# Performance work log

Hardware: AMD Instinct MI355X
Metric: run time of the kernel (lower is better)

The kernel has to match this reference:

```python
import jax, jax.numpy as jnp
import numpy as np

IN_DIM, BANDS = 42, 22
H_VAD, H_NOISE, H_DEN = 24, 48, 96


def gru(x, w_ih, w_hh, b_ih, b_hh):
    """torch.nn.GRU (batch_first) semantics, h0=0.
    x: [B,T,D]; w_ih: [3H,D]; w_hh: [3H,H]; gate order r,z,n."""
    H = w_hh.shape[1]
    # precompute input projections for all timesteps (big GEMM, recurrence only on H)
    xp = jnp.einsum('btd,gd->btg', x, w_ih) + b_ih  # [B,T,3H]

    def step(h, xt):
        hp = h @ w_hh.T + b_hh
        xr, xz, xn = jnp.split(xt, 3, axis=-1)
        hr, hz, hn = jnp.split(hp, 3, axis=-1)
        r = jax.nn.sigmoid(xr + hr)
        z = jax.nn.sigmoid(xz + hz)
        n = jnp.tanh(xn + r * hn)
        h_new = (1.0 - z) * n + z * h
        return h_new, h_new

    h0 = jnp.zeros((x.shape[0], H), x.dtype)
    _, hs = jax.lax.scan(step, h0, jnp.swapaxes(xp, 0, 1))  # [T,B,H]
    return jnp.swapaxes(hs, 0, 1)  # [B,T,H]


def setup_inputs() -> dict:
    key = jax.random.key(0)
    ks = jax.random.split(key, 20)

    def w(k, shape, fan):
        return (jax.random.normal(k, shape, jnp.float32) / np.sqrt(fan)).astype(jnp.float32)

    B, T = 256, 2000
    d_noise_in = H_VAD + H_VAD + IN_DIM     # 90
    d_den_in = H_VAD + H_NOISE + IN_DIM     # 114
    return {
        'x': jax.random.normal(ks[0], (B, T, IN_DIM), jnp.float32),
        'in_w': w(ks[1], (H_VAD, IN_DIM), IN_DIM),
        'in_b': jnp.zeros((H_VAD,), jnp.float32),
        'vad_wih': w(ks[2], (3 * H_VAD, H_VAD), H_VAD),
        'vad_whh': w(ks[3], (3 * H_VAD, H_VAD), H_VAD),
        'vad_bih': jnp.zeros((3 * H_VAD,), jnp.float32),
        'vad_bhh': jnp.zeros((3 * H_VAD,), jnp.float32),
        'vad_out_w': w(ks[4], (1, H_VAD), H_VAD),
        'vad_out_b': jnp.zeros((1,), jnp.float32),
        'noise_wih': w(ks[5], (3 * H_NOISE, d_noise_in), d_noise_in),
        'noise_whh': w(ks[6], (3 * H_NOISE, H_NOISE), H_NOISE),
        'noise_bih': jnp.zeros((3 * H_NOISE,), jnp.float32),
        'noise_bhh': jnp.zeros((3 * H_NOISE,), jnp.float32),
        'den_wih': w(ks[7], (3 * H_DEN, d_den_in), d_den_in),
        'den_whh': w(ks[8], (3 * H_DEN, H_DEN), H_DEN),
        'den_bih': jnp.zeros((3 * H_DEN,), jnp.float32),
        'den_bhh': jnp.zeros((3 * H_DEN,), jnp.float32),
        'out_w': w(ks[9], (BANDS, H_DEN), H_DEN),
        'out_b': jnp.zeros((BANDS,), jnp.float32),
    }


def reference(x, in_w, in_b, vad_wih, vad_whh, vad_bih, vad_bhh,
              vad_out_w, vad_out_b, noise_wih, noise_whh, noise_bih, noise_bhh,
              den_wih, den_whh, den_bih, den_bhh, out_w, out_b):
    tmp = jnp.tanh(jnp.einsum('btd,hd->bth', x, in_w) + in_b)          # [B,T,24]
    vad_h = gru(tmp, vad_wih, vad_whh, vad_bih, vad_bhh)               # [B,T,24]
    vad = jax.nn.sigmoid(jnp.einsum('bth,oh->bto', vad_h, vad_out_w) + vad_out_b)
    noise_in = jnp.concatenate([tmp, vad_h, x], axis=-1)               # [B,T,90]
    noise_h = gru(noise_in, noise_wih, noise_whh, noise_bih, noise_bhh)  # [B,T,48]
    den_in = jnp.concatenate([vad_h, noise_h, x], axis=-1)             # [B,T,114]
    den_h = gru(den_in, den_wih, den_whh, den_bih, den_bhh)            # [B,T,96]
    gains = jax.nn.sigmoid(jnp.einsum('bth,oh->bto', den_h, out_w) + out_b)
    return gains, vad
```

## Files before the change

kernel.cpp:

```cpp
#include <hip/hip_runtime.h>

typedef _Float16 f16;
typedef _Float16 h2 __attribute__((ext_vector_type(2)));
typedef unsigned int u32;

#define TB  256
#define TTT 2000
#define INW 42
#define HV  24
#define HN  48
#define HD  96
#define NTH 640

__device__ __forceinline__ float fsigm(float v) {
    return __builtin_amdgcn_rcpf(1.0f + __builtin_amdgcn_exp2f(-1.44269504089f * v));
}
__device__ __forceinline__ float ftanh(float v) {
    float e = __builtin_amdgcn_exp2f(2.88539008178f * v);
    return 1.0f - 2.0f * __builtin_amdgcn_rcpf(e + 1.0f);
}
__device__ __forceinline__ float dot2f(u32 a, u32 w, float c) {
#if __has_builtin(__builtin_amdgcn_fdot2)
    return __builtin_amdgcn_fdot2(__builtin_bit_cast(h2, a), __builtin_bit_cast(h2, w), c, false);
#else
    h2 av = __builtin_bit_cast(h2, a), wv = __builtin_bit_cast(h2, w);
    return c + (float)av[0] * (float)wv[0] + (float)av[1] * (float)wv[1];
#endif
}
__device__ __forceinline__ u32 packw(float a, float b) {
    h2 v; v[0] = (f16)a; v[1] = (f16)b;
    return __builtin_bit_cast(u32, v);
}
template<int CTRL>
__device__ __forceinline__ float dpp_add(float x) {
    int y = __builtin_amdgcn_mov_dpp(__builtin_bit_cast(int, x), CTRL, 0xF, 0xF, true);
    return x + __builtin_bit_cast(float, y);
}

#define SYNCB() asm volatile("s_waitcnt lgkmcnt(0)\n\ts_barrier" ::: "memory")

#define ACCI(AV, W, IDX) do { u32 _a = (AV); \
    rr = dot2f(_a, W[0][IDX], rr); zz = dot2f(_a, W[1][IDX], zz); an = dot2f(_a, W[2][IDX], an); } while (0)
#define ACCH(AV, W, IDX) do { u32 _a = (AV); \
    rr = dot2f(_a, W[0][IDX], rr); zz = dot2f(_a, W[1][IDX], zz); hn = dot2f(_a, W[2][IDX], hn); } while (0)
#define RED4_Q() do { \
    rr = dpp_add<0xB1>(rr); rr = dpp_add<0x4E>(rr); \
    zz = dpp_add<0xB1>(zz); zz = dpp_add<0x4E>(zz); \
    an = dpp_add<0xB1>(an); an = dpp_add<0x4E>(an); \
    hn = dpp_add<0xB1>(hn); hn = dpp_add<0x4E>(hn); } while (0)
#define RED4_1() do { \
    rr = dpp_add<0xB1>(rr); zz = dpp_add<0xB1>(zz); \
    an = dpp_add<0xB1>(an); hn = dpp_add<0xB1>(hn); } while (0)

template<int N> struct IC { static constexpr int val = N; };

__global__ __launch_bounds__(NTH, 3) void rnnoise_kernel(
    const float* __restrict__ gx,
    const float* __restrict__ in_w,      const float* __restrict__ in_b,
    const float* __restrict__ vad_wih,   const float* __restrict__ vad_whh,
    const float* __restrict__ vad_bih,   const float* __restrict__ vad_bhh,
    const float* __restrict__ vad_out_w, const float* __restrict__ vad_out_b,
    const float* __restrict__ noise_wih, const float* __restrict__ noise_whh,
    const float* __restrict__ noise_bih, const float* __restrict__ noise_bhh,
    const float* __restrict__ den_wih,   const float* __restrict__ den_whh,
    const float* __restrict__ den_bih,   const float* __restrict__ den_bhh,
    const float* __restrict__ out_w,     const float* __restrict__ out_b,
    float* __restrict__ gains, float* __restrict__ vout)
{
    __shared__ __align__(16) f16 s_x[4][48];
    __shared__ __align__(16) f16 s_tmp[4][24];
    __shared__ __align__(16) f16 s_vadh[4][24];
    __shared__ __align__(16) f16 s_noih[4][48];
    __shared__ __align__(16) f16 s_denh[4][96];

    const int tid  = threadIdx.x;
    const int wid  = tid >> 6;
    const int lane = tid & 63;
    const int b    = blockIdx.x;

    if (tid < 96)  ((u32*)s_x)[tid]    = 0u;
    if (tid < 48)  ((u32*)s_tmp)[tid]  = 0u;
    if (tid < 48)  ((u32*)s_vadh)[tid] = 0u;
    if (tid < 96)  ((u32*)s_noih)[tid] = 0u;
    if (tid < 192) ((u32*)s_denh)[tid] = 0u;
    __syncthreads();

    const int role = (wid == 9) ? 2 : ((wid == 4 || wid == 5 || wid == 8) ? 1 : 0);

    if (role == 0) {
        const int dwi = (wid < 4) ? wid : (wid - 2);
        const int u = dwi * 16 + (lane >> 2), q = lane & 3;
        u32 wdh[3][12], wdx[3][6], wdv[3][3], wdn[3][6];
        #pragma unroll
        for (int g = 0; g < 3; ++g) {
            const float* wr = den_whh + (g * HD + u) * HD + 24 * q;
            #pragma unroll
            for (int j = 0; j < 12; ++j) wdh[g][j] = packw(wr[2*j], wr[2*j+1]);
            const float* wi = den_wih + (g * HD + u) * 114;
            #pragma unroll
            for (int j = 0; j < 6; ++j) {
                int c0 = 12*q + 2*j;
                float a = (c0     < INW) ? wi[72 + c0]     : 0.f;
                float c = (c0 + 1 < INW) ? wi[72 + c0 + 1] : 0.f;
                wdx[g][j] = packw(a, c);
            }
            #pragma unroll
            for (int j = 0; j < 3; ++j) wdv[g][j] = packw(wi[6*q + 2*j], wi[6*q + 2*j + 1]);
            #pragma unroll
            for (int j = 0; j < 6; ++j) wdn[g][j] = packw(wi[24 + 12*q + 2*j], wi[24 + 12*q + 2*j + 1]);
        }
        const float bdr  = den_bih[u]      + den_bhh[u];
        const float bdz  = den_bih[HD+u]   + den_bhh[HD+u];
        const float bdni = den_bih[2*HD+u];
        const float bdnh = den_bhh[2*HD+u];
        float hreg = 0.f;

        auto step = [&](auto PC, int k) {
            constexpr int P  = decltype(PC)::val;
            constexpr int SI = (P + 1) & 3;
            if (k >= 3 && k <= TTT + 2) {
                float rr = 0, zz = 0, an = 0, hn = 0;
                const uint4* hp = (const uint4*)&s_denh[P][24*q];
                #pragma unroll
                for (int v = 0; v < 3; ++v) {
                    uint4 a = hp[v];
                    ACCH(a.x, wdh, 4*v+0); ACCH(a.y, wdh, 4*v+1);
                    ACCH(a.z, wdh, 4*v+2); ACCH(a.w, wdh, 4*v+3);
                }
                const uint2* xp = (const uint2*)&s_x[SI][12*q];
                #pragma unroll
                for (int v = 0; v < 3; ++v) { uint2 a = xp[v]; ACCI(a.x, wdx, 2*v); ACCI(a.y, wdx, 2*v+1); }
                const u32* vp = (const u32*)&s_vadh[SI][6*q];
                #pragma unroll
                for (int v = 0; v < 3; ++v) ACCI(vp[v], wdv, v);
                const uint2* np = (const uint2*)&s_noih[SI][12*q];
                #pragma unroll
                for (int v = 0; v < 3; ++v) { uint2 a = np[v]; ACCI(a.x, wdn, 2*v); ACCI(a.y, wdn, 2*v+1); }
                RED4_Q();
                if (q == 0) {
                    float r = fsigm(rr + bdr);
                    float z = fsigm(zz + bdz);
                    float n = ftanh(an + bdni + r * (hn + bdnh));
                    hreg = z * (hreg - n) + n;
                    s_denh[SI][u] = (f16)hreg;
                }
            }
            SYNCB();
        };
        #pragma clang loop unroll(disable)
        for (int k0 = 0; k0 < TTT + 4; k0 += 4) {
            step(IC<0>{}, k0); step(IC<1>{}, k0+1); step(IC<2>{}, k0+2); step(IC<3>{}, k0+3);
        }

    } else if (role == 1) {
        const int nwi = (wid == 4) ? 0 : ((wid == 5) ? 1 : 2);
        const int L = nwi * 64 + lane, u = L >> 2, q = L & 3;
        const int o = L >> 3, s8 = L & 7;
        const int oc = (o < 22) ? o : 0;
        u32 wnh[3][6], wnt[3][3], wnv[3][3], wnx[3][6], wo[6];
        #pragma unroll
        for (int g = 0; g < 3; ++g) {
            const float* wr = noise_whh + (g * HN + u) * HN + 12 * q;
            #pragma unroll
            for (int j = 0; j < 6; ++j) wnh[g][j] = packw(wr[2*j], wr[2*j+1]);
            const float* wi = noise_wih + (g * HN + u) * 90;
            #pragma unroll
            for (int j = 0; j < 3; ++j) wnt[g][j] = packw(wi[6*q + 2*j], wi[6*q + 2*j + 1]);
            #pragma unroll
            for (int j = 0; j < 3; ++j) wnv[g][j] = packw(wi[24 + 6*q + 2*j], wi[24 + 6*q + 2*j + 1]);
            #pragma unroll
            for (int j = 0; j < 6; ++j) {
                int c0 = 12*q + 2*j;
                float a = (c0     < INW) ? wi[48 + c0]     : 0.f;
                float c = (c0 + 1 < INW) ? wi[48 + c0 + 1] : 0.f;
                wnx[g][j] = packw(a, c);
            }
        }
        #pragma unroll
        for (int j = 0; j < 6; ++j) wo[j] = packw(out_w[oc*HD + 12*s8 + 2*j], out_w[oc*HD + 12*s8 + 2*j + 1]);
        const float bnr  = noise_bih[u]    + noise_bhh[u];
        const float bnz  = noise_bih[HN+u] + noise_bhh[HN+u];
        const float bnni = noise_bih[2*HN+u];
        const float bnnh = noise_bhh[2*HN+u];
        const float bo   = out_b[oc];
        float hreg = 0.f;

        auto step = [&](auto PC, int k) {
            constexpr int P  = decltype(PC)::val;
            constexpr int SI = (P + 2) & 3;
            constexpr int SH = (P + 1) & 3;
            if (k >= 2 && k <= TTT + 1) {
                float rr = 0, zz = 0, an = 0, hn = 0;
                const uint2* hp = (const uint2*)&s_noih[SH][12*q];
                #pragma unroll
                for (int v = 0; v < 3; ++v) { uint2 a = hp[v]; ACCH(a.x, wnh, 2*v); ACCH(a.y, wnh, 2*v+1); }
                const u32* tp = (const u32*)&s_tmp[SI][6*q];
                #pragma unroll
                for (int v = 0; v < 3; ++v) ACCI(tp[v], wnt, v);
                const u32* vp = (const u32*)&s_vadh[SI][6*q];
                #pragma unroll
                for (int v = 0; v < 3; ++v) ACCI(vp[v], wnv, v);
                const uint2* xp = (const uint2*)&s_x[SI][12*q];
                #pragma unroll
                for (int v = 0; v < 3; ++v) { uint2 a = xp[v]; ACCI(a.x, wnx, 2*v); ACCI(a.y, wnx, 2*v+1); }
                RED4_Q();
                if (q == 0) {
                    float r = fsigm(rr + bnr);
                    float z = fsigm(zz + bnz);
                    float n = ftanh(an + bnni + r * (hn + bnnh));
                    hreg = z * (hreg - n) + n;
                    s_noih[SI][u] = (f16)hreg;
                }
            }
            if (k >= 4) {
                float acc = 0;
                const uint2* dp = (const uint2*)&s_denh[P][12*s8];
                #pragma unroll
                for (int v = 0; v < 3; ++v) {
                    uint2 a = dp[v];
                    acc = dot2f(a.x, wo[2*v], acc); acc = dot2f(a.y, wo[2*v+1], acc);
                }
                acc = dpp_add<0xB1>(acc); acc = dpp_add<0x4E>(acc);
                acc += __shfl_xor(acc, 4);
                if (s8 == 0 && o < 22)
                    gains[((size_t)b * TTT + (k - 4)) * 22 + o] = fsigm(acc + bo);
            }
            SYNCB();
        };
        #pragma clang loop unroll(disable)
        for (int k0 = 0; k0 < TTT + 4; k0 += 4) {
            step(IC<0>{}, k0); step(IC<1>{}, k0+1); step(IC<2>{}, k0+2); step(IC<3>{}, k0+3);
        }

    } else {
        const int l = lane;
        const int u = (l < 48) ? (l >> 1) : 0, q2 = l & 1;
        u32 wvi[3][6], wvh[3][6], wtm[12];
        float bvr = 0, bvz = 0, bvni = 0, bvnh = 0, btm = 0, wvo_u = 0;
        if (l < 48) {
            #pragma unroll
            for (int g = 0; g < 3; ++g) {
                const float* wi = vad_wih + (g * HV + u) * HV + 12 * q2;
                const float* wh = vad_whh + (g * HV + u) * HV + 12 * q2;
                #pragma unroll
                for (int j = 0; j < 6; ++j) {
                    wvi[g][j] = packw(wi[2*j], wi[2*j+1]);
                    wvh[g][j] = packw(wh[2*j], wh[2*j+1]);
                }
            }
            #pragma unroll
            for (int j = 0; j < 12; ++j) {
                int c0 = 24*q2 + 2*j;
                float a = (c0     < INW) ? in_w[u*INW + c0]     : 0.f;
                float c = (c0 + 1 < INW) ? in_w[u*INW + c0 + 1] : 0.f;
                wtm[j] = packw(a, c);
            }
            bvr  = vad_bih[u]      + vad_bhh[u];
            bvz  = vad_bih[HV+u]   + vad_bhh[HV+u];
            bvni = vad_bih[2*HV+u];
            bvnh = vad_bhh[2*HV+u];
            btm  = in_b[u];
            if (q2 == 0) wvo_u = vad_out_w[u];
        }
        const float bvo = vad_out_b[0];
        float hreg = 0.f;

        float xa = 0, xb = 0, xc = 0, xd = 0;
        if (l < INW) {
            xa = gx[((size_t)b * TTT + 0) * INW + l];
            xb = gx[((size_t)b * TTT + 1) * INW + l];
            xc = gx[((size_t)b * TTT + 2) * INW + l];
            xd = gx[((size_t)b * TTT + 3) * INW + l];
        }

        auto step = [&](auto PC, int k) {
            constexpr int P  = decltype(PC)::val;
            constexpr int ST = (P + 3) & 3;
            constexpr int SH = (P + 2) & 3;
            if (k < TTT && l < INW) {
                float xv;
                if constexpr (P == 0) xv = xa; else if constexpr (P == 1) xv = xb;
                else if constexpr (P == 2) xv = xc; else xv = xd;
                s_x[P][l] = (f16)xv;
            }
            if (k + 4 < TTT && l < INW) {
                float xv = gx[((size_t)b * TTT + (k + 4)) * INW + l];
                if constexpr (P == 0) xa = xv; else if constexpr (P == 1) xb = xv;
                else if constexpr (P == 2) xc = xv; else xd = xv;
            }
            if (k >= 1 && k <= TTT) {
                float rr = 0, zz = 0, an = 0, hn = 0;
                if (l < 48) {
                    const uint2* tp = (const uint2*)&s_tmp[ST][12*q2];
                    const uint2* hp = (const uint2*)&s_vadh[SH][12*q2];
                    #pragma unroll
                    for (int v = 0; v < 3; ++v) {
                        uint2 a = tp[v]; ACCI(a.x, wvi, 2*v); ACCI(a.y, wvi, 2*v+1);
                        uint2 h = hp[v]; ACCH(h.x, wvh, 2*v); ACCH(h.y, wvh, 2*v+1);
                    }
                    RED4_1();
                    if (q2 == 0) {
                        float r = fsigm(rr + bvr);
                        float z = fsigm(zz + bvz);
                        float n = ftanh(an + bvni + r * (hn + bvnh));
                        hreg = z * (hreg - n) + n;
                        s_vadh[ST][u] = (f16)hreg;
                    }
                }
                float val = (l < 48 && q2 == 0) ? (wvo_u * hreg) : 0.f;
                val = dpp_add<0xB1>(val); val = dpp_add<0x4E>(val);
                val += __shfl_xor(val, 4); val += __shfl_xor(val, 8);
                val += __shfl_xor(val, 16); val += __shfl_xor(val, 32);
                if (l == 0) vout[(size_t)b * TTT + (k - 1)] = fsigm(val + bvo);
            }
            if (k < TTT) {
                float acc = 0;
                if (l < 48) {
                    const uint4* xp = (const uint4*)&s_x[P][24*q2];
                    #pragma unroll
                    for (int v = 0; v < 3; ++v) {
                        uint4 a = xp[v];
                        acc = dot2f(a.x, wtm[4*v+0], acc); acc = dot2f(a.y, wtm[4*v+1], acc);
                        acc = dot2f(a.z, wtm[4*v+2], acc); acc = dot2f(a.w, wtm[4*v+3], acc);
                    }
                    acc = dpp_add<0xB1>(acc);
                    if (q2 == 0) s_tmp[P][u] = (f16)ftanh(acc + btm);
                }
            }
            SYNCB();
        };
        #pragma clang loop unroll(disable)
        for (int k0 = 0; k0 < TTT + 4; k0 += 4) {
            step(IC<0>{}, k0); step(IC<1>{}, k0+1); step(IC<2>{}, k0+2); step(IC<3>{}, k0+3);
        }
    }
}

extern "C" void kernel_launch(void* const* d_in, const int* in_sizes, int n_in,
                              void* d_out, int out_size, void* d_ws, size_t ws_size,
                              hipStream_t stream) {
    (void)in_sizes; (void)n_in; (void)d_ws; (void)ws_size; (void)out_size;
    const float* gx        = (const float*)d_in[0];
    const float* in_w      = (const float*)d_in[1];
    const float* in_b      = (const float*)d_in[2];
    const float* vad_wih   = (const float*)d_in[3];
    const float* vad_whh   = (const float*)d_in[4];
    const float* vad_bih   = (const float*)d_in[5];
    const float* vad_bhh   = (const float*)d_in[6];
    const float* vad_out_w = (const float*)d_in[7];
    const float* vad_out_b = (const float*)d_in[8];
    const float* noise_wih = (const float*)d_in[9];
    const float* noise_whh = (const float*)d_in[10];
    const float* noise_bih = (const float*)d_in[11];
    const float* noise_bhh = (const float*)d_in[12];
    const float* den_wih   = (const float*)d_in[13];
    const float* den_whh   = (const float*)d_in[14];
    const float* den_bih   = (const float*)d_in[15];
    const float* den_bhh   = (const float*)d_in[16];
    const float* out_w     = (const float*)d_in[17];
    const float* out_b     = (const float*)d_in[18];
    float* gains = (float*)d_out;
    float* vout  = (float*)d_out + (size_t)TB * (size_t)TTT * 22;

    rnnoise_kernel<<<dim3(TB), dim3(NTH), 0, stream>>>(
        gx, in_w, in_b, vad_wih, vad_whh, vad_bih, vad_bhh, vad_out_w, vad_out_b,
        noise_wih, noise_whh, noise_bih, noise_bhh, den_wih, den_whh, den_bih, den_bhh,
        out_w, out_b, gains, vout);
}
```

Baseline: 1.923 ms.

## Restructure wavefront pipeline with 8-deep ring buffer and contiguous concatenated input rows

Replaces the separate per-tensor shared buffers with one 8-slot ring of packed activation rows, laid out so that the noise and denoise GRU inputs are contiguous concatenations. Each input projection then becomes a single vectorised read. The pipeline depth grows from 4 to 8 stages and the next-step input loads are prefetched into registers one step ahead. The input dense layer and x loading move from the VAD wave to a denoise wave, and the gains output moves from the noise waves to another denoise wave, with launch bounds relaxed to one block per CU. The aim is to shorten the per-step critical path and balance work across waves, at the cost of more registers and added latency from the deeper pipeline.

```diff
diff --git a/kernel.cpp b/kernel.cpp
--- a/kernel.cpp
+++ b/kernel.cpp
@@ -12,6 +12,12 @@
 #define HD  96
 #define NTH 640
 
+#define R_N   0
+#define R_NH  96
+#define R_D   160
+#define R_DH  288
+#define ACTW  384
+
 __device__ __forceinline__ float fsigm(float v) {
     return __builtin_amdgcn_rcpf(1.0f + __builtin_amdgcn_exp2f(-1.44269504089f * v));
 }
@@ -43,6 +49,13 @@
     rr = dot2f(_a, W[0][IDX], rr); zz = dot2f(_a, W[1][IDX], zz); an = dot2f(_a, W[2][IDX], an); } while (0)
 #define ACCH(AV, W, IDX) do { u32 _a = (AV); \
     rr = dot2f(_a, W[0][IDX], rr); zz = dot2f(_a, W[1][IDX], zz); hn = dot2f(_a, W[2][IDX], hn); } while (0)
+#define ACCI4(U4, W, M0) do { uint4 _u4 = (U4); \
+    ACCI(_u4.x, W, (M0)+0); ACCI(_u4.y, W, (M0)+1); ACCI(_u4.z, W, (M0)+2); ACCI(_u4.w, W, (M0)+3); } while (0)
+#define ACCH4(U4, W, M0) do { uint4 _u4 = (U4); \
+    ACCH(_u4.x, W, (M0)+0); ACCH(_u4.y, W, (M0)+1); ACCH(_u4.z, W, (M0)+2); ACCH(_u4.w, W, (M0)+3); } while (0)
+#define OACC4(U4, W, M0) do { uint4 _u4 = (U4); \
+    acc = dot2f(_u4.x, W[(M0)+0], acc); acc = dot2f(_u4.y, W[(M0)+1], acc); \
+    acc = dot2f(_u4.z, W[(M0)+2], acc); acc = dot2f(_u4.w, W[(M0)+3], acc); } while (0)
 #define RED4_Q() do { \
     rr = dpp_add<0xB1>(rr); rr = dpp_add<0x4E>(rr); \
     zz = dpp_add<0xB1>(zz); zz = dpp_add<0x4E>(zz); \
@@ -54,7 +67,7 @@
 
 template<int N> struct IC { static constexpr int val = N; };
 
-__global__ __launch_bounds__(NTH, 3) void rnnoise_kernel(
+__global__ __launch_bounds__(NTH, 1) void rnnoise_kernel(
     const float* __restrict__ gx,
     const float* __restrict__ in_w,      const float* __restrict__ in_b,
     const float* __restrict__ vad_wih,   const float* __restrict__ vad_whh,
@@ -67,232 +80,256 @@
     const float* __restrict__ out_w,     const float* __restrict__ out_b,
     float* __restrict__ gains, float* __restrict__ vout)
 {
-    __shared__ __align__(16) f16 s_x[4][48];
-    __shared__ __align__(16) f16 s_tmp[4][24];
-    __shared__ __align__(16) f16 s_vadh[4][24];
-    __shared__ __align__(16) f16 s_noih[4][48];
-    __shared__ __align__(16) f16 s_denh[4][96];
-
-    const int tid  = threadIdx.x;
-    const int wid  = tid >> 6;
-    const int lane = tid & 63;
-    const int b    = blockIdx.x;
-
-    if (tid < 96)  ((u32*)s_x)[tid]    = 0u;
-    if (tid < 48)  ((u32*)s_tmp)[tid]  = 0u;
-    if (tid < 48)  ((u32*)s_vadh)[tid] = 0u;
-    if (tid < 96)  ((u32*)s_noih)[tid] = 0u;
-    if (tid < 192) ((u32*)s_denh)[tid] = 0u;
+    __shared__ __align__(16) f16 act[8][ACTW];
+
+    const int tid = threadIdx.x, wid = tid >> 6, lane = tid & 63;
+    const int b = blockIdx.x;
+
+    #pragma unroll
+    for (int i = 0; i < 3; ++i) {
+        int idx = tid + i * NTH;
+        if (idx < 8 * ACTW / 2) ((u32*)act)[idx] = 0u;
+    }
     __syncthreads();
 
-    const int role = (wid == 9) ? 2 : ((wid == 4 || wid == 5 || wid == 8) ? 1 : 0);
-
-    if (role == 0) {
+    const bool is_vad = (wid == 9);
+    const bool is_noi = (wid == 4 || wid == 5 || wid == 8);
+
+    if (!is_vad && !is_noi) {
         const int dwi = (wid < 4) ? wid : (wid - 2);
-        const int u = dwi * 16 + (lane >> 2), q = lane & 3;
-        u32 wdh[3][12], wdx[3][6], wdv[3][3], wdn[3][6];
+        const int u = 16 * dwi + (lane >> 2), q = lane & 3;
+        const bool w6 = (wid == 6), w7 = (wid == 7);
+
+        u32 wdi[3][16], wdh[3][12];
         #pragma unroll
         for (int g = 0; g < 3; ++g) {
-            const float* wr = den_whh + (g * HD + u) * HD + 24 * q;
-            #pragma unroll
-            for (int j = 0; j < 12; ++j) wdh[g][j] = packw(wr[2*j], wr[2*j+1]);
             const float* wi = den_wih + (g * HD + u) * 114;
             #pragma unroll
-            for (int j = 0; j < 6; ++j) {
-                int c0 = 12*q + 2*j;
-                float a = (c0     < INW) ? wi[72 + c0]     : 0.f;
-                float c = (c0 + 1 < INW) ? wi[72 + c0 + 1] : 0.f;
-                wdx[g][j] = packw(a, c);
-            }
-            #pragma unroll
-            for (int j = 0; j < 3; ++j) wdv[g][j] = packw(wi[6*q + 2*j], wi[6*q + 2*j + 1]);
-            #pragma unroll
-            for (int j = 0; j < 6; ++j) wdn[g][j] = packw(wi[24 + 12*q + 2*j], wi[24 + 12*q + 2*j + 1]);
-        }
-        const float bdr  = den_bih[u]      + den_bhh[u];
-        const float bdz  = den_bih[HD+u]   + den_bhh[HD+u];
-        const float bdni = den_bih[2*HD+u];
-        const float bdnh = den_bhh[2*HD+u];
+            for (int m = 0; m < 16; ++m) {
+                int c = 32 * q + 2 * m;
+                float a  = (c     < 114) ? wi[c]     : 0.f;
+                float b2 = (c + 1 < 114) ? wi[c + 1] : 0.f;
+                wdi[g][m] = packw(a, b2);
+            }
+            const float* wh = den_whh + (g * HD + u) * HD + 24 * q;
+            #pragma unroll
+            for (int m = 0; m < 12; ++m) wdh[g][m] = packw(wh[2*m], wh[2*m+1]);
+        }
+        const float bdr  = den_bih[u]        + den_bhh[u];
+        const float bdz  = den_bih[HD + u]   + den_bhh[HD + u];
+        const float bdni = den_bih[2*HD + u];
+        const float bdnh = den_bhh[2*HD + u];
+
+        const int o = lane >> 1, jo = lane & 1;
+        const int oc = (o < 22) ? o : 0;
+        u32 wo[24]; float bo = 0.f;
+        if (w7) {
+            #pragma unroll
+            for (int m = 0; m < 24; ++m)
+                wo[m] = packw(out_w[oc * HD + 48 * jo + 2*m], out_w[oc * HD + 48 * jo + 2*m + 1]);
+            bo = out_b[oc];
+        }
+        const int ut = (lane < 48) ? (lane >> 1) : 0, q2t = lane & 1;
+        u32 wtm[12]; float btm = 0.f;
+        float x0=0,x1=0,x2=0,x3=0,x4=0,x5=0,x6=0,x7=0;
+        if (w6) {
+            #pragma unroll
+            for (int m = 0; m < 12; ++m) {
+                int c = 24 * q2t + 2 * m;
+                float a  = (c     < INW) ? in_w[ut * INW + c]     : 0.f;
+                float b2 = (c + 1 < INW) ? in_w[ut * INW + c + 1] : 0.f;
+                wtm[m] = packw(a, b2);
+            }
+            btm = in_b[ut];
+            if (lane < INW) {
+                x0 = gx[((size_t)b*TTT + 0)*INW + lane]; x1 = gx[((size_t)b*TTT + 1)*INW + lane];
+                x2 = gx[((size_t)b*TTT + 2)*INW + lane]; x3 = gx[((size_t)b*TTT + 3)*INW + lane];
+                x4 = gx[((size_t)b*TTT + 4)*INW + lane]; x5 = gx[((size_t)b*TTT + 5)*INW + lane];
+                x6 = gx[((size_t)b*TTT + 6)*INW + lane]; x7 = gx[((size_t)b*TTT + 7)*INW + lane];
+            }
+        }
         float hreg = 0.f;
+        uint4 pfA0{}, pfA1{}, pfA2{}, pfA3{}, pfB0{}, pfB1{}, pfB2{}, pfB3{};
 
         auto step = [&](auto PC, int k) {
-            constexpr int P  = decltype(PC)::val;
-            constexpr int SI = (P + 1) & 3;
-            if (k >= 3 && k <= TTT + 2) {
-                float rr = 0, zz = 0, an = 0, hn = 0;
-                const uint4* hp = (const uint4*)&s_denh[P][24*q];
-                #pragma unroll
-                for (int v = 0; v < 3; ++v) {
-                    uint4 a = hp[v];
-                    ACCH(a.x, wdh, 4*v+0); ACCH(a.y, wdh, 4*v+1);
-                    ACCH(a.z, wdh, 4*v+2); ACCH(a.w, wdh, 4*v+3);
+            constexpr int P = decltype(PC)::val;
+            constexpr int SHH = (P + 2) & 7;
+            constexpr int SCU = (P + 3) & 7;
+            constexpr int SPF = (P + 4) & 7;
+            constexpr int SOT = (P + 1) & 7;
+            if (w6 && k < TTT && lane < INW) {
+                float xv;
+                if constexpr (P==0) xv=x0; else if constexpr (P==1) xv=x1;
+                else if constexpr (P==2) xv=x2; else if constexpr (P==3) xv=x3;
+                else if constexpr (P==4) xv=x4; else if constexpr (P==5) xv=x5;
+                else if constexpr (P==6) xv=x6; else xv=x7;
+                f16 xh = (f16)xv;
+                act[P][R_N + 48 + lane] = xh;
+                act[P][R_D + 72 + lane] = xh;
+            }
+            const uint4* hp = (const uint4*)&act[SHH][R_DH + 24 * q];
+            uint4 h0 = hp[0], h1 = hp[1], h2 = hp[2];
+            uint4 e0{}, e1{}, e2{}, e3{}, e4{}, e5{};
+            if (w7) {
+                const uint4* ep = (const uint4*)&act[SOT][R_DH + 48 * jo];
+                e0=ep[0]; e1=ep[1]; e2=ep[2]; e3=ep[3]; e4=ep[4]; e5=ep[5];
+            }
+            {
+                const uint4* dp = (const uint4*)&act[SPF][R_D + 32 * q];
+                if constexpr ((P & 1) == 0) { pfB0=dp[0]; pfB1=dp[1]; pfB2=dp[2]; pfB3=dp[3]; }
+                else                        { pfA0=dp[0]; pfA1=dp[1]; pfA2=dp[2]; pfA3=dp[3]; }
+            }
+            float rr=0, zz=0, an=0, hn=0;
+            {
+                uint4 a0=(P&1)?pfB0:pfA0, a1=(P&1)?pfB1:pfA1, a2=(P&1)?pfB2:pfA2, a3=(P&1)?pfB3:pfA3;
+                ACCI4(a0, wdi, 0); ACCI4(a1, wdi, 4); ACCI4(a2, wdi, 8); ACCI4(a3, wdi, 12);
+            }
+            ACCH4(h0, wdh, 0); ACCH4(h1, wdh, 4); ACCH4(h2, wdh, 8);
+            RED4_Q();
+            if (k >= 5 && k < TTT + 5 && q == 0) {
+                float r = fsigm(rr + bdr);
+                float z = fsigm(zz + bdz);
+                float n = ftanh(an + bdni + r * (hn + bdnh));
+                hreg = z * (hreg - n) + n;
+                act[SCU][R_DH + u] = (f16)hreg;
+            }
+            if (w7 && k >= 7 && k < TTT + 7) {
+                float acc = 0;
+                OACC4(e0, wo, 0); OACC4(e1, wo, 4); OACC4(e2, wo, 8);
+                OACC4(e3, wo, 12); OACC4(e4, wo, 16); OACC4(e5, wo, 20);
+                acc += __shfl_xor(acc, 1);
+                if (jo == 0 && o < 22)
+                    gains[((size_t)b * TTT + (k - 7)) * 22 + o] = fsigm(acc + bo);
+            }
+            if (w6) {
+                if (k + 8 < TTT && lane < INW) {
+                    float xv = gx[((size_t)b * TTT + (k + 8)) * INW + lane];
+                    if constexpr (P==0) x0=xv; else if constexpr (P==1) x1=xv;
+                    else if constexpr (P==2) x2=xv; else if constexpr (P==3) x3=xv;
+                    else if constexpr (P==4) x4=xv; else if constexpr (P==5) x5=xv;
+                    else if constexpr (P==6) x6=xv; else x7=xv;
                 }
-                const uint2* xp = (const uint2*)&s_x[SI][12*q];
-                #pragma unroll
-                for (int v = 0; v < 3; ++v) { uint2 a = xp[v]; ACCI(a.x, wdx, 2*v); ACCI(a.y, wdx, 2*v+1); }
-                const u32* vp = (const u32*)&s_vadh[SI][6*q];
-                #pragma unroll
-                for (int v = 0; v < 3; ++v) ACCI(vp[v], wdv, v);
-                const uint2* np = (const uint2*)&s_noih[SI][12*q];
-                #pragma unroll
-                for (int v = 0; v < 3; ++v) { uint2 a = np[v]; ACCI(a.x, wdn, 2*v); ACCI(a.y, wdn, 2*v+1); }
-                RED4_Q();
-                if (q == 0) {
-                    float r = fsigm(rr + bdr);
-                    float z = fsigm(zz + bdz);
-                    float n = ftanh(an + bdni + r * (hn + bdnh));
-                    hreg = z * (hreg - n) + n;
-                    s_denh[SI][u] = (f16)hreg;
+                if (k < TTT && lane < 48) {
+                    float acc = 0;
+                    const uint4* xp = (const uint4*)&act[P][R_N + 48 + 24 * q2t];
+                    uint4 a = xp[0], b2 = xp[1], c2 = xp[2];
+                    acc=dot2f(a.x,wtm[0],acc);  acc=dot2f(a.y,wtm[1],acc);
+                    acc=dot2f(a.z,wtm[2],acc);  acc=dot2f(a.w,wtm[3],acc);
+                    acc=dot2f(b2.x,wtm[4],acc); acc=dot2f(b2.y,wtm[5],acc);
+                    acc=dot2f(b2.z,wtm[6],acc); acc=dot2f(b2.w,wtm[7],acc);
+                    acc=dot2f(c2.x,wtm[8],acc); acc=dot2f(c2.y,wtm[9],acc);
+                    acc=dot2f(c2.z,wtm[10],acc);acc=dot2f(c2.w,wtm[11],acc);
+                    acc = dpp_add<0xB1>(acc);
+                    if (q2t == 0) act[P][R_N + ut] = (f16)ftanh(acc + btm);
                 }
             }
             SYNCB();
         };
         #pragma clang loop unroll(disable)
-        for (int k0 = 0; k0 < TTT + 4; k0 += 4) {
-            step(IC<0>{}, k0); step(IC<1>{}, k0+1); step(IC<2>{}, k0+2); step(IC<3>{}, k0+3);
-        }
-
-    } else if (role == 1) {
+        for (int k0 = 0; k0 < TTT + 8; k0 += 8) {
+            step(IC<0>{},k0);   step(IC<1>{},k0+1); step(IC<2>{},k0+2); step(IC<3>{},k0+3);
+            step(IC<4>{},k0+4); step(IC<5>{},k0+5); step(IC<6>{},k0+6); step(IC<7>{},k0+7);
+        }
+
+    } else if (is_noi) {
         const int nwi = (wid == 4) ? 0 : ((wid == 5) ? 1 : 2);
-        const int L = nwi * 64 + lane, u = L >> 2, q = L & 3;
-        const int o = L >> 3, s8 = L & 7;
-        const int oc = (o < 22) ? o : 0;
-        u32 wnh[3][6], wnt[3][3], wnv[3][3], wnx[3][6], wo[6];
+        const int u = 16 * nwi + (lane >> 2), q = lane & 3;
+        u32 wni[3][12], wnh[3][8];
         #pragma unroll
         for (int g = 0; g < 3; ++g) {
-            const float* wr = noise_whh + (g * HN + u) * HN + 12 * q;
-            #pragma unroll
-            for (int j = 0; j < 6; ++j) wnh[g][j] = packw(wr[2*j], wr[2*j+1]);
             const float* wi = noise_wih + (g * HN + u) * 90;
             #pragma unroll
-            for (int j = 0; j < 3; ++j) wnt[g][j] = packw(wi[6*q + 2*j], wi[6*q + 2*j + 1]);
-            #pragma unroll
-            for (int j = 0; j < 3; ++j) wnv[g][j] = packw(wi[24 + 6*q + 2*j], wi[24 + 6*q + 2*j + 1]);
-            #pragma unroll
-            for (int j = 0; j < 6; ++j) {
-                int c0 = 12*q + 2*j;
-                float a = (c0     < INW) ? wi[48 + c0]     : 0.f;
-                float c = (c0 + 1 < INW) ? wi[48 + c0 + 1] : 0.f;
-                wnx[g][j] = packw(a, c);
-            }
-        }
-        #pragma unroll
-        for (int j = 0; j < 6; ++j) wo[j] = packw(out_w[oc*HD + 12*s8 + 2*j], out_w[oc*HD + 12*s8 + 2*j + 1]);
-        const float bnr  = noise_bih[u]    + noise_bhh[u];
-        const float bnz  = noise_bih[HN+u] + noise_bhh[HN+u];
-        const float bnni = noise_bih[2*HN+u];
-        const float bnnh = noise_bhh[2*HN+u];
-        const float bo   = out_b[oc];
+            for (int m = 0; m < 12; ++m) {
+                int c = 24 * q + 2 * m;
+                float a  = (c     < 90) ? wi[c]     : 0.f;
+                float b2 = (c + 1 < 90) ? wi[c + 1] : 0.f;
+                wni[g][m] = packw(a, b2);
+            }
+            const float* wh = noise_whh + (g * HN + u) * HN;
+            #pragma unroll
+            for (int m = 0; m < 8; ++m) {
+                int c = 16 * q + 2 * m;
+                float a  = (c     < 48) ? wh[c]     : 0.f;
+                float b2 = (c + 1 < 48) ? wh[c + 1] : 0.f;
+                wnh[g][m] = packw(a, b2);
+            }
+        }
+        const float bnr  = noise_bih[u]        + noise_bhh[u];
+        const float bnz  = noise_bih[HN + u]   + noise_bhh[HN + u];
+        const float bnni = noise_bih[2*HN + u];
+        const float bnnh = noise_bhh[2*HN + u];
         float hreg = 0.f;
+        uint4 pfA0{}, pfA1{}, pfA2{}, pfB0{}, pfB1{}, pfB2{};
 
         auto step = [&](auto PC, int k) {
-            constexpr int P  = decltype(PC)::val;
-            constexpr int SI = (P + 2) & 3;
-            constexpr int SH = (P + 1) & 3;
-            if (k >= 2 && k <= TTT + 1) {
-                float rr = 0, zz = 0, an = 0, hn = 0;
-                const uint2* hp = (const uint2*)&s_noih[SH][12*q];
-                #pragma unroll
-                for (int v = 0; v < 3; ++v) { uint2 a = hp[v]; ACCH(a.x, wnh, 2*v); ACCH(a.y, wnh, 2*v+1); }
-                const u32* tp = (const u32*)&s_tmp[SI][6*q];
-                #pragma unroll
-                for (int v = 0; v < 3; ++v) ACCI(tp[v], wnt, v);
-                const u32* vp = (const u32*)&s_vadh[SI][6*q];
-                #pragma unroll
-                for (int v = 0; v < 3; ++v) ACCI(vp[v], wnv, v);
-                const uint2* xp = (const uint2*)&s_x[SI][12*q];
-                #pragma unroll
-                for (int v = 0; v < 3; ++v) { uint2 a = xp[v]; ACCI(a.x, wnx, 2*v); ACCI(a.y, wnx, 2*v+1); }
-                RED4_Q();
-                if (q == 0) {
-                    float r = fsigm(rr + bnr);
-                    float z = fsigm(zz + bnz);
-                    float n = ftanh(an + bnni + r * (hn + bnnh));
-                    hreg = z * (hreg - n) + n;
-                    s_noih[SI][u] = (f16)hreg;
-                }
-            }
-            if (k >= 4) {
-                float acc = 0;
-                const uint2* dp = (const uint2*)&s_denh[P][12*s8];
-                #pragma unroll
-                for (int v = 0; v < 3; ++v) {
-                    uint2 a = dp[v];
-                    acc = dot2f(a.x, wo[2*v], acc); acc = dot2f(a.y, wo[2*v+1], acc);
-                }
-                acc = dpp_add<0xB1>(acc); acc = dpp_add<0x4E>(acc);
-                acc += __shfl_xor(acc, 4);
-                if (s8 == 0 && o < 22)
-                    gains[((size_t)b * TTT + (k - 4)) * 22 + o] = fsigm(acc + bo);
+            constexpr int P = decltype(PC)::val;
+            constexpr int SHH = (P + 4) & 7;
+            constexpr int SCU = (P + 5) & 7;
+            constexpr int SPF = (P + 6) & 7;
+            const uint4* hp = (const uint4*)&act[SHH][R_NH + 16 * q];
+            uint4 h0 = hp[0], h1 = hp[1];
+            {
+                const uint4* np = (const uint4*)&act[SPF][R_N + 24 * q];
+                if constexpr ((P & 1) == 0) { pfB0=np[0]; pfB1=np[1]; pfB2=np[2]; }
+                else                        { pfA0=np[0]; pfA1=np[1]; pfA2=np[2]; }
+            }
+            float rr=0, zz=0, an=0, hn=0;
+            {
+                uint4 a0=(P&1)?pfB0:pfA0, a1=(P&1)?pfB1:pfA1, a2=(P&1)?pfB2:pfA2;
+                ACCI4(a0, wni, 0); ACCI4(a1, wni, 4); ACCI4(a2, wni, 8);
+            }
+            ACCH4(h0, wnh, 0); ACCH4(h1, wnh, 4);
+            RED4_Q();
+            if (k >= 3 && k < TTT + 3 && q == 0) {
+                float r = fsigm(rr + bnr);
+                float z = fsigm(zz + bnz);
+                float n = ftanh(an + bnni + r * (hn + bnnh));
+                hreg = z * (hreg - n) + n;
+                f16 hh = (f16)hreg;
+                act[SCU][R_NH + u]     = hh;
+                act[SCU][R_D + 24 + u] = hh;
             }
             SYNCB();
         };
         #pragma clang loop unroll(disable)
-        for (int k0 = 0; k0 < TTT + 4; k0 += 4) {
-            step(IC<0>{}, k0); step(IC<1>{}, k0+1); step(IC<2>{}, k0+2); step(IC<3>{}, k0+3);
+        for (int k0 = 0; k0 < TTT + 8; k0 += 8) {
+            step(IC<0>{},k0);   step(IC<1>{},k0+1); step(IC<2>{},k0+2); step(IC<3>{},k0+3);
+            step(IC<4>{},k0+4); step(IC<5>{},k0+5); step(IC<6>{},k0+6); step(IC<7>{},k0+7);
         }
 
     } else {
-        const int l = lane;
-        const int u = (l < 48) ? (l >> 1) : 0, q2 = l & 1;
-        u32 wvi[3][6], wvh[3][6], wtm[12];
-        float bvr = 0, bvz = 0, bvni = 0, bvnh = 0, btm = 0, wvo_u = 0;
-        if (l < 48) {
+        const int uv = (lane < 48) ? (lane >> 1) : 0, q2 = lane & 1;
+        u32 wvi[3][6], wvh[3][6];
+        float bvr=0, bvz=0, bvni=0, bvnh=0, wvo_u=0;
+        if (lane < 48) {
             #pragma unroll
             for (int g = 0; g < 3; ++g) {
-                const float* wi = vad_wih + (g * HV + u) * HV + 12 * q2;
-                const float* wh = vad_whh + (g * HV + u) * HV + 12 * q2;
+                const float* wi = vad_wih + (g * HV + uv) * HV + 12 * q2;
+                const float* wh = vad_whh + (g * HV + uv) * HV + 12 * q2;
                 #pragma unroll
                 for (int j = 0; j < 6; ++j) {
                     wvi[g][j] = packw(wi[2*j], wi[2*j+1]);
                     wvh[g][j] = packw(wh[2*j], wh[2*j+1]);
                 }
             }
-            #pragma unroll
-            for (int j = 0; j < 12; ++j) {
-                int c0 = 24*q2 + 2*j;
-                float a = (c0     < INW) ? in_w[u*INW + c0]     : 0.f;
-                float c = (c0 + 1 < INW) ? in_w[u*INW + c0 + 1] : 0.f;
-                wtm[j] = packw(a, c);
-            }
-            bvr  = vad_bih[u]      + vad_bhh[u];
-            bvz  = vad_bih[HV+u]   + vad_bhh[HV+u];
-            bvni = vad_bih[2*HV+u];
-            bvnh = vad_bhh[2*HV+u];
-            btm  = in_b[u];
-            if (q2 == 0) wvo_u = vad_out_w[u];
+            bvr  = vad_bih[uv]        + vad_bhh[uv];
+            bvz  = vad_bih[HV + uv]   + vad_bhh[HV + uv];
+            bvni = vad_bih[2*HV + uv];
+            bvnh = vad_bhh[2*HV + uv];
+            if (q2 == 0) wvo_u = vad_out_w[uv];
         }
         const float bvo = vad_out_b[0];
         float hreg = 0.f;
 
-        float xa = 0, xb = 0, xc = 0, xd = 0;
-        if (l < INW) {
-            xa = gx[((size_t)b * TTT + 0) * INW + l];
-            xb = gx[((size_t)b * TTT + 1) * INW + l];
-            xc = gx[((size_t)b * TTT + 2) * INW + l];
-            xd = gx[((size_t)b * TTT + 3) * INW + l];
-        }
-
         auto step = [&](auto PC, int k) {
-            constexpr int P  = decltype(PC)::val;
-            constexpr int ST = (P + 3) & 3;
-            constexpr int SH = (P + 2) & 3;
-            if (k < TTT && l < INW) {
-                float xv;
-                if constexpr (P == 0) xv = xa; else if constexpr (P == 1) xv = xb;
-                else if constexpr (P == 2) xv = xc; else xv = xd;
-                s_x[P][l] = (f16)xv;
-            }
-            if (k + 4 < TTT && l < INW) {
-                float xv = gx[((size_t)b * TTT + (k + 4)) * INW + l];
-                if constexpr (P == 0) xa = xv; else if constexpr (P == 1) xb = xv;
-                else if constexpr (P == 2) xc = xv; else xd = xv;
-            }
+            constexpr int P = decltype(PC)::val;
+            constexpr int ST  = (P + 7) & 7;
+            constexpr int SVH = (P + 6) & 7;
             if (k >= 1 && k <= TTT) {
-                float rr = 0, zz = 0, an = 0, hn = 0;
-                if (l < 48) {
-                    const uint2* tp = (const uint2*)&s_tmp[ST][12*q2];
-                    const uint2* hp = (const uint2*)&s_vadh[SH][12*q2];
+                float rr=0, zz=0, an=0, hn=0;
+                if (lane < 48) {
+                    const uint2* tp = (const uint2*)&act[ST][R_N + 12 * q2];
+                    const uint2* hp = (const uint2*)&act[SVH][R_N + 24 + 12 * q2];
                     #pragma unroll
                     for (int v = 0; v < 3; ++v) {
                         uint2 a = tp[v]; ACCI(a.x, wvi, 2*v); ACCI(a.y, wvi, 2*v+1);
@@ -304,34 +341,23 @@
                         float z = fsigm(zz + bvz);
                         float n = ftanh(an + bvni + r * (hn + bvnh));
                         hreg = z * (hreg - n) + n;
-                        s_vadh[ST][u] = (f16)hreg;
+                        f16 hh = (f16)hreg;
+                        act[ST][R_N + 24 + uv] = hh;
+                        act[ST][R_D + uv]      = hh;
                     }
                 }
-                float val = (l < 48 && q2 == 0) ? (wvo_u * hreg) : 0.f;
+                float val = (lane < 48 && q2 == 0) ? (wvo_u * hreg) : 0.f;
                 val = dpp_add<0xB1>(val); val = dpp_add<0x4E>(val);
-                val += __shfl_xor(val, 4); val += __shfl_xor(val, 8);
+                val += __shfl_xor(val, 4);  val += __shfl_xor(val, 8);
                 val += __shfl_xor(val, 16); val += __shfl_xor(val, 32);
-                if (l == 0) vout[(size_t)b * TTT + (k - 1)] = fsigm(val + bvo);
-            }
-            if (k < TTT) {
-                float acc = 0;
-                if (l < 48) {
-                    const uint4* xp = (const uint4*)&s_x[P][24*q2];
-                    #pragma unroll
-                    for (int v = 0; v < 3; ++v) {
-                        uint4 a = xp[v];
-                        acc = dot2f(a.x, wtm[4*v+0], acc); acc = dot2f(a.y, wtm[4*v+1], acc);
-                        acc = dot2f(a.z, wtm[4*v+2], acc); acc = dot2f(a.w, wtm[4*v+3], acc);
-                    }
-                    acc = dpp_add<0xB1>(acc);
-                    if (q2 == 0) s_tmp[P][u] = (f16)ftanh(acc + btm);
-                }
+                if (lane == 0) vout[(size_t)b * TTT + (k - 1)] = fsigm(val + bvo);
             }
             SYNCB();
         };
         #pragma clang loop unroll(disable)
-        for (int k0 = 0; k0 < TTT + 4; k0 += 4) {
-            step(IC<0>{}, k0); step(IC<1>{}, k0+1); step(IC<2>{}, k0+2); step(IC<3>{}, k0+3);
+        for (int k0 = 0; k0 < TTT + 8; k0 += 8) {
+            step(IC<0>{},k0);   step(IC<1>{},k0+1); step(IC<2>{},k0+2); step(IC<3>{},k0+3);
+            step(IC<4>{},k0+4); step(IC<5>{},k0+5); step(IC<6>{},k0+6); step(IC<7>{},k0+7);
         }
     }
 }
```

New measurement: 4.540 ms. 2.36x slower.

## Pack GRU activations into contiguous concatenated LDS rows for wide loads

Applied to the files above, without the earlier changes.

Replaces the separate per-tensor shared buffers with one activation array per pipeline slot. Each GRU's concatenated input (vad_h|noise_h|x for den, tmp|vad_h|x for noise) sits contiguously, so the dot products issue a few 16-byte LDS reads instead of many scattered small ones. Producers now write duplicate copies of each hidden state and x into both layouts, which adds LDS stores. The noise warps are remapped per wave, two shuffle steps in the vad reduction become DPP row shifts, and launch bounds drop from 3 to 2 blocks per CU to allow more registers.

```diff
diff --git a/kernel.cpp b/kernel.cpp
--- a/kernel.cpp
+++ b/kernel.cpp
@@ -12,6 +12,12 @@
 #define HD  96
 #define NTH 640
 
+#define DIN 0
+#define DH  128
+#define NIN 224
+#define NH  320
+#define ACTW 384
+
 __device__ __forceinline__ float fsigm(float v) {
     return __builtin_amdgcn_rcpf(1.0f + __builtin_amdgcn_exp2f(-1.44269504089f * v));
 }
@@ -43,6 +49,10 @@
     rr = dot2f(_a, W[0][IDX], rr); zz = dot2f(_a, W[1][IDX], zz); an = dot2f(_a, W[2][IDX], an); } while (0)
 #define ACCH(AV, W, IDX) do { u32 _a = (AV); \
     rr = dot2f(_a, W[0][IDX], rr); zz = dot2f(_a, W[1][IDX], zz); hn = dot2f(_a, W[2][IDX], hn); } while (0)
+#define ACCI4(U4, W, M0) do { uint4 _u4 = (U4); \
+    ACCI(_u4.x, W, (M0)+0); ACCI(_u4.y, W, (M0)+1); ACCI(_u4.z, W, (M0)+2); ACCI(_u4.w, W, (M0)+3); } while (0)
+#define ACCH4(U4, W, M0) do { uint4 _u4 = (U4); \
+    ACCH(_u4.x, W, (M0)+0); ACCH(_u4.y, W, (M0)+1); ACCH(_u4.z, W, (M0)+2); ACCH(_u4.w, W, (M0)+3); } while (0)
 #define RED4_Q() do { \
     rr = dpp_add<0xB1>(rr); rr = dpp_add<0x4E>(rr); \
     zz = dpp_add<0xB1>(zz); zz = dpp_add<0x4E>(zz); \
@@ -54,7 +64,7 @@
 
 template<int N> struct IC { static constexpr int val = N; };
 
-__global__ __launch_bounds__(NTH, 3) void rnnoise_kernel(
+__global__ __launch_bounds__(NTH, 2) void rnnoise_kernel(
     const float* __restrict__ gx,
     const float* __restrict__ in_w,      const float* __restrict__ in_b,
     const float* __restrict__ vad_wih,   const float* __restrict__ vad_whh,
@@ -67,52 +77,39 @@
     const float* __restrict__ out_w,     const float* __restrict__ out_b,
     float* __restrict__ gains, float* __restrict__ vout)
 {
-    __shared__ __align__(16) f16 s_x[4][48];
-    __shared__ __align__(16) f16 s_tmp[4][24];
-    __shared__ __align__(16) f16 s_vadh[4][24];
-    __shared__ __align__(16) f16 s_noih[4][48];
-    __shared__ __align__(16) f16 s_denh[4][96];
-
-    const int tid  = threadIdx.x;
-    const int wid  = tid >> 6;
-    const int lane = tid & 63;
-    const int b    = blockIdx.x;
-
-    if (tid < 96)  ((u32*)s_x)[tid]    = 0u;
-    if (tid < 48)  ((u32*)s_tmp)[tid]  = 0u;
-    if (tid < 48)  ((u32*)s_vadh)[tid] = 0u;
-    if (tid < 96)  ((u32*)s_noih)[tid] = 0u;
-    if (tid < 192) ((u32*)s_denh)[tid] = 0u;
+    __shared__ __align__(16) f16 act[4][ACTW];
+
+    const int tid = threadIdx.x, wid = tid >> 6, lane = tid & 63;
+    const int b = blockIdx.x;
+
+    if (tid < 768) ((u32*)act)[tid] = 0u;
+    if (tid + NTH < 768) ((u32*)act)[tid + NTH] = 0u;
     __syncthreads();
 
     const int role = (wid == 9) ? 2 : ((wid == 4 || wid == 5 || wid == 8) ? 1 : 0);
 
     if (role == 0) {
         const int dwi = (wid < 4) ? wid : (wid - 2);
-        const int u = dwi * 16 + (lane >> 2), q = lane & 3;
-        u32 wdh[3][12], wdx[3][6], wdv[3][3], wdn[3][6];
+        const int u = 16 * dwi + (lane >> 2), q = lane & 3;
+        u32 wdi[3][16], wdh[3][12];
         #pragma unroll
         for (int g = 0; g < 3; ++g) {
-            const float* wr = den_whh + (g * HD + u) * HD + 24 * q;
-            #pragma unroll
-            for (int j = 0; j < 12; ++j) wdh[g][j] = packw(wr[2*j], wr[2*j+1]);
             const float* wi = den_wih + (g * HD + u) * 114;
             #pragma unroll
-            for (int j = 0; j < 6; ++j) {
-                int c0 = 12*q + 2*j;
-                float a = (c0     < INW) ? wi[72 + c0]     : 0.f;
-                float c = (c0 + 1 < INW) ? wi[72 + c0 + 1] : 0.f;
-                wdx[g][j] = packw(a, c);
-            }
-            #pragma unroll
-            for (int j = 0; j < 3; ++j) wdv[g][j] = packw(wi[6*q + 2*j], wi[6*q + 2*j + 1]);
-            #pragma unroll
-            for (int j = 0; j < 6; ++j) wdn[g][j] = packw(wi[24 + 12*q + 2*j], wi[24 + 12*q + 2*j + 1]);
-        }
-        const float bdr  = den_bih[u]      + den_bhh[u];
-        const float bdz  = den_bih[HD+u]   + den_bhh[HD+u];
-        const float bdni = den_bih[2*HD+u];
-        const float bdnh = den_bhh[2*HD+u];
+            for (int m = 0; m < 16; ++m) {
+                int c = 32 * q + 2 * m;
+                float a  = (c     < 114) ? wi[c]     : 0.f;
+                float b2 = (c + 1 < 114) ? wi[c + 1] : 0.f;
+                wdi[g][m] = packw(a, b2);
+            }
+            const float* wh = den_whh + (g * HD + u) * HD + 24 * q;
+            #pragma unroll
+            for (int m = 0; m < 12; ++m) wdh[g][m] = packw(wh[2*m], wh[2*m+1]);
+        }
+        const float bdr  = den_bih[u]        + den_bhh[u];
+        const float bdz  = den_bih[HD + u]   + den_bhh[HD + u];
+        const float bdni = den_bih[2*HD + u];
+        const float bdnh = den_bhh[2*HD + u];
         float hreg = 0.f;
 
         auto step = [&](auto PC, int k) {
@@ -120,29 +117,19 @@
             constexpr int SI = (P + 1) & 3;
             if (k >= 3 && k <= TTT + 2) {
                 float rr = 0, zz = 0, an = 0, hn = 0;
-                const uint4* hp = (const uint4*)&s_denh[P][24*q];
-                #pragma unroll
-                for (int v = 0; v < 3; ++v) {
-                    uint4 a = hp[v];
-                    ACCH(a.x, wdh, 4*v+0); ACCH(a.y, wdh, 4*v+1);
-                    ACCH(a.z, wdh, 4*v+2); ACCH(a.w, wdh, 4*v+3);
-                }
-                const uint2* xp = (const uint2*)&s_x[SI][12*q];
-                #pragma unroll
-                for (int v = 0; v < 3; ++v) { uint2 a = xp[v]; ACCI(a.x, wdx, 2*v); ACCI(a.y, wdx, 2*v+1); }
-                const u32* vp = (const u32*)&s_vadh[SI][6*q];
-                #pragma unroll
-                for (int v = 0; v < 3; ++v) ACCI(vp[v], wdv, v);
-                const uint2* np = (const uint2*)&s_noih[SI][12*q];
-                #pragma unroll
-                for (int v = 0; v < 3; ++v) { uint2 a = np[v]; ACCI(a.x, wdn, 2*v); ACCI(a.y, wdn, 2*v+1); }
+                const uint4* hp = (const uint4*)&act[P][DH + 24 * q];
+                uint4 h0 = hp[0], h1 = hp[1], h2 = hp[2];
+                const uint4* ip = (const uint4*)&act[SI][DIN + 32 * q];
+                uint4 a0 = ip[0], a1 = ip[1], a2 = ip[2], a3 = ip[3];
+                ACCI4(a0, wdi, 0); ACCI4(a1, wdi, 4); ACCI4(a2, wdi, 8); ACCI4(a3, wdi, 12);
+                ACCH4(h0, wdh, 0); ACCH4(h1, wdh, 4); ACCH4(h2, wdh, 8);
                 RED4_Q();
                 if (q == 0) {
                     float r = fsigm(rr + bdr);
                     float z = fsigm(zz + bdz);
                     float n = ftanh(an + bdni + r * (hn + bdnh));
                     hreg = z * (hreg - n) + n;
-                    s_denh[SI][u] = (f16)hreg;
+                    act[SI][DH + u] = (f16)hreg;
                 }
             }
             SYNCB();
@@ -154,72 +141,69 @@
 
     } else if (role == 1) {
         const int nwi = (wid == 4) ? 0 : ((wid == 5) ? 1 : 2);
-        const int L = nwi * 64 + lane, u = L >> 2, q = L & 3;
-        const int o = L >> 3, s8 = L & 7;
+        const int u = 16 * nwi + (lane >> 2), q = lane & 3;
+        const int o = 8 * nwi + (lane >> 3), s8 = lane & 7;
         const int oc = (o < 22) ? o : 0;
-        u32 wnh[3][6], wnt[3][3], wnv[3][3], wnx[3][6], wo[6];
+        u32 wni[3][12], wnh[3][8], wo[6];
         #pragma unroll
         for (int g = 0; g < 3; ++g) {
-            const float* wr = noise_whh + (g * HN + u) * HN + 12 * q;
-            #pragma unroll
-            for (int j = 0; j < 6; ++j) wnh[g][j] = packw(wr[2*j], wr[2*j+1]);
             const float* wi = noise_wih + (g * HN + u) * 90;
             #pragma unroll
-            for (int j = 0; j < 3; ++j) wnt[g][j] = packw(wi[6*q + 2*j], wi[6*q + 2*j + 1]);
-            #pragma unroll
-            for (int j = 0; j < 3; ++j) wnv[g][j] = packw(wi[24 + 6*q + 2*j], wi[24 + 6*q + 2*j + 1]);
-            #pragma unroll
-            for (int j = 0; j < 6; ++j) {
-                int c0 = 12*q + 2*j;
-                float a = (c0     < INW) ? wi[48 + c0]     : 0.f;
-                float c = (c0 + 1 < INW) ? wi[48 + c0 + 1] : 0.f;
-                wnx[g][j] = packw(a, c);
+            for (int m = 0; m < 12; ++m) {
+                int c = 24 * q + 2 * m;
+                float a  = (c     < 90) ? wi[c]     : 0.f;
+                float b2 = (c + 1 < 90) ? wi[c + 1] : 0.f;
+                wni[g][m] = packw(a, b2);
+            }
+            const float* wh = noise_whh + (g * HN + u) * HN;
+            #pragma unroll
+            for (int m = 0; m < 8; ++m) {
+                int c = 16 * q + 2 * m;
+                float a  = (c     < 48) ? wh[c]     : 0.f;
+                float b2 = (c + 1 < 48) ? wh[c + 1] : 0.f;
+                wnh[g][m] = packw(a, b2);
             }
         }
         #pragma unroll
-        for (int j = 0; j < 6; ++j) wo[j] = packw(out_w[oc*HD + 12*s8 + 2*j], out_w[oc*HD + 12*s8 + 2*j + 1]);
-        const float bnr  = noise_bih[u]    + noise_bhh[u];
-        const float bnz  = noise_bih[HN+u] + noise_bhh[HN+u];
-        const float bnni = noise_bih[2*HN+u];
-        const float bnnh = noise_bhh[2*HN+u];
+        for (int m = 0; m < 6; ++m)
+            wo[m] = packw(out_w[oc*HD + 12*s8 + 2*m], out_w[oc*HD + 12*s8 + 2*m + 1]);
+        const float bnr  = noise_bih[u]        + noise_bhh[u];
+        const float bnz  = noise_bih[HN + u]   + noise_bhh[HN + u];
+        const float bnni = noise_bih[2*HN + u];
+        const float bnnh = noise_bhh[2*HN + u];
         const float bo   = out_b[oc];
         float hreg = 0.f;
 
         auto step = [&](auto PC, int k) {
-            constexpr int P  = decltype(PC)::val;
-            constexpr int SI = (P + 2) & 3;
-            constexpr int SH = (P + 1) & 3;
+            constexpr int P   = decltype(PC)::val;
+            constexpr int SI  = (P + 2) & 3;
+            constexpr int SH  = (P + 1) & 3;
             if (k >= 2 && k <= TTT + 1) {
                 float rr = 0, zz = 0, an = 0, hn = 0;
-                const uint2* hp = (const uint2*)&s_noih[SH][12*q];
-                #pragma unroll
-                for (int v = 0; v < 3; ++v) { uint2 a = hp[v]; ACCH(a.x, wnh, 2*v); ACCH(a.y, wnh, 2*v+1); }
-                const u32* tp = (const u32*)&s_tmp[SI][6*q];
-                #pragma unroll
-                for (int v = 0; v < 3; ++v) ACCI(tp[v], wnt, v);
-                const u32* vp = (const u32*)&s_vadh[SI][6*q];
-                #pragma unroll
-                for (int v = 0; v < 3; ++v) ACCI(vp[v], wnv, v);
-                const uint2* xp = (const uint2*)&s_x[SI][12*q];
-                #pragma unroll
-                for (int v = 0; v < 3; ++v) { uint2 a = xp[v]; ACCI(a.x, wnx, 2*v); ACCI(a.y, wnx, 2*v+1); }
+                const uint4* hp = (const uint4*)&act[SH][NH + 16 * q];
+                uint4 h0 = hp[0], h1 = hp[1];
+                const uint4* ip = (const uint4*)&act[SI][NIN + 24 * q];
+                uint4 a0 = ip[0], a1 = ip[1], a2 = ip[2];
+                ACCI4(a0, wni, 0); ACCI4(a1, wni, 4); ACCI4(a2, wni, 8);
+                ACCH4(h0, wnh, 0); ACCH4(h1, wnh, 4);
                 RED4_Q();
                 if (q == 0) {
                     float r = fsigm(rr + bnr);
                     float z = fsigm(zz + bnz);
                     float n = ftanh(an + bnni + r * (hn + bnnh));
                     hreg = z * (hreg - n) + n;
-                    s_noih[SI][u] = (f16)hreg;
+                    f16 hh = (f16)hreg;
+                    act[SI][NH + u]       = hh;
+                    act[SI][DIN + 24 + u] = hh;
                 }
             }
             if (k >= 4) {
                 float acc = 0;
-                const uint2* dp = (const uint2*)&s_denh[P][12*s8];
-                #pragma unroll
-                for (int v = 0; v < 3; ++v) {
-                    uint2 a = dp[v];
-                    acc = dot2f(a.x, wo[2*v], acc); acc = dot2f(a.y, wo[2*v+1], acc);
-                }
+                const uint2* dp = (const uint2*)&act[P][DH + 12 * s8];
+                uint2 d0 = dp[0], d1 = dp[1], d2 = dp[2];
+                acc = dot2f(d0.x, wo[0], acc); acc = dot2f(d0.y, wo[1], acc);
+                acc = dot2f(d1.x, wo[2], acc); acc = dot2f(d1.y, wo[3], acc);
+                acc = dot2f(d2.x, wo[4], acc); acc = dot2f(d2.y, wo[5], acc);
                 acc = dpp_add<0xB1>(acc); acc = dpp_add<0x4E>(acc);
                 acc += __shfl_xor(acc, 4);
                 if (s8 == 0 && o < 22)
@@ -250,15 +234,15 @@
             }
             #pragma unroll
             for (int j = 0; j < 12; ++j) {
-                int c0 = 24*q2 + 2*j;
-                float a = (c0     < INW) ? in_w[u*INW + c0]     : 0.f;
-                float c = (c0 + 1 < INW) ? in_w[u*INW + c0 + 1] : 0.f;
+                int c0 = 24 * q2 + 2 * j;
+                float a = (c0     < INW) ? in_w[u * INW + c0]     : 0.f;
+                float c = (c0 + 1 < INW) ? in_w[u * INW + c0 + 1] : 0.f;
                 wtm[j] = packw(a, c);
             }
-            bvr  = vad_bih[u]      + vad_bhh[u];
-            bvz  = vad_bih[HV+u]   + vad_bhh[HV+u];
-            bvni = vad_bih[2*HV+u];
-            bvnh = vad_bhh[2*HV+u];
+            bvr  = vad_bih[u]        + vad_bhh[u];
+            bvz  = vad_bih[HV + u]   + vad_bhh[HV + u];
+            bvni = vad_bih[2*HV + u];
+            bvnh = vad_bhh[2*HV + u];
             btm  = in_b[u];
             if (q2 == 0) wvo_u = vad_out_w[u];
         }
@@ -281,7 +265,9 @@
                 float xv;
                 if constexpr (P == 0) xv = xa; else if constexpr (P == 1) xv = xb;
                 else if constexpr (P == 2) xv = xc; else xv = xd;
-                s_x[P][l] = (f16)xv;
+                f16 xh = (f16)xv;
+                act[P][NIN + 48 + l] = xh;
+                act[P][DIN + 72 + l] = xh;
             }
             if (k + 4 < TTT && l < INW) {
                 float xv = gx[((size_t)b * TTT + (k + 4)) * INW + l];
@@ -291,8 +277,8 @@
             if (k >= 1 && k <= TTT) {
                 float rr = 0, zz = 0, an = 0, hn = 0;
                 if (l < 48) {
-                    const uint2* tp = (const uint2*)&s_tmp[ST][12*q2];
-                    const uint2* hp = (const uint2*)&s_vadh[SH][12*q2];
+                    const uint2* tp = (const uint2*)&act[ST][NIN + 12 * q2];
+                    const uint2* hp = (const uint2*)&act[SH][NIN + 24 + 12 * q2];
                     #pragma unroll
                     for (int v = 0; v < 3; ++v) {
                         uint2 a = tp[v]; ACCI(a.x, wvi, 2*v); ACCI(a.y, wvi, 2*v+1);
@@ -304,28 +290,29 @@
                         float z = fsigm(zz + bvz);
                         float n = ftanh(an + bvni + r * (hn + bvnh));
                         hreg = z * (hreg - n) + n;
-                        s_vadh[ST][u] = (f16)hreg;
+                        f16 hh = (f16)hreg;
+                        act[ST][NIN + 24 + u] = hh;
+                        act[ST][DIN + u]      = hh;
                     }
                 }
                 float val = (l < 48 && q2 == 0) ? (wvo_u * hreg) : 0.f;
-                val = dpp_add<0xB1>(val); val = dpp_add<0x4E>(val);
-                val += __shfl_xor(val, 4); val += __shfl_xor(val, 8);
+                val = dpp_add<0xB1>(val);  val = dpp_add<0x4E>(val);
+                val = dpp_add<0x124>(val); val = dpp_add<0x128>(val);
                 val += __shfl_xor(val, 16); val += __shfl_xor(val, 32);
                 if (l == 0) vout[(size_t)b * TTT + (k - 1)] = fsigm(val + bvo);
             }
-            if (k < TTT) {
+            if (k < TTT && l < 48) {
                 float acc = 0;
-                if (l < 48) {
-                    const uint4* xp = (const uint4*)&s_x[P][24*q2];
-                    #pragma unroll
-                    for (int v = 0; v < 3; ++v) {
-                        uint4 a = xp[v];
-                        acc = dot2f(a.x, wtm[4*v+0], acc); acc = dot2f(a.y, wtm[4*v+1], acc);
-                        acc = dot2f(a.z, wtm[4*v+2], acc); acc = dot2f(a.w, wtm[4*v+3], acc);
-                    }
-                    acc = dpp_add<0xB1>(acc);
-                    if (q2 == 0) s_tmp[P][u] = (f16)ftanh(acc + btm);
-                }
+                const uint4* xp = (const uint4*)&act[P][NIN + 48 + 24 * q2];
+                uint4 a = xp[0], b2 = xp[1], c2 = xp[2];
+                acc = dot2f(a.x,  wtm[0], acc);  acc = dot2f(a.y,  wtm[1], acc);
+                acc = dot2f(a.z,  wtm[2], acc);  acc = dot2f(a.w,  wtm[3], acc);
+                acc = dot2f(b2.x, wtm[4], acc);  acc = dot2f(b2.y, wtm[5], acc);
+                acc = dot2f(b2.z, wtm[6], acc);  acc = dot2f(b2.w, wtm[7], acc);
+                acc = dot2f(c2.x, wtm[8], acc);  acc = dot2f(c2.y, wtm[9], acc);
+                acc = dot2f(c2.z, wtm[10], acc); acc = dot2f(c2.w, wtm[11], acc);
+                acc = dpp_add<0xB1>(acc);
+                if (q2 == 0) act[P][NIN + u] = (f16)ftanh(acc + btm);
             }
             SYNCB();
         };
```

After: 1.893 ms. Within noise of the previous version (-1.6%).
